# Kernel tuning notes

Hardware: AMD Instinct MI355X
Metric: run time of the kernel (lower is better)

## Reference

```python
import jax, jax.numpy as jnp
import numpy as np

N = 512           # nodes
DIM = 64          # feature dim (in_dim == dim)
KS = (0.9, 0.7, 0.6)
M_DIM = 17
EDGE_DIM = 1
EIN = 2 * DIM + 1 + EDGE_DIM  # EGNN edge-mlp input width = 130
L = 3             # shared EGNN layers per scale


def _rn(k, shape, s=0.05):
    return jax.random.normal(k, shape, jnp.float32) * s


def setup_inputs() -> dict:
    key = jax.random.key(0)
    k = jax.random.split(key, 12)
    feat = jax.random.normal(k[0], (1, N, DIM), jnp.float32)
    coor = jax.random.normal(k[1], (1, N, 3), jnp.float32)
    # sparse-ish binary adjacency stored densely, as the module expects
    edge = (jax.random.uniform(k[2], (1, N, N, 1)) < 0.05).astype(jnp.float32)
    return {
        "feat": feat, "coor": coor, "edge": edge,
        "We1": _rn(k[3], (L, EIN, 2 * EIN)), "be1": jnp.zeros((L, 2 * EIN), jnp.float32),
        "We2": _rn(k[4], (L, 2 * EIN, M_DIM)), "be2": jnp.zeros((L, M_DIM), jnp.float32),
        "Wc1": _rn(k[5], (L, M_DIM, 4 * M_DIM)), "bc1": jnp.zeros((L, 4 * M_DIM), jnp.float32),
        "Wc2": _rn(k[6], (L, 4 * M_DIM, 1)), "bc2": jnp.zeros((L, 1), jnp.float32),
        "Wn1": _rn(k[7], (L, DIM + M_DIM, 2 * DIM)), "bn1": jnp.zeros((L, 2 * DIM), jnp.float32),
        "Wn2": _rn(k[8], (L, 2 * DIM, DIM)), "bn2": jnp.zeros((L, DIM), jnp.float32),
        "wp": _rn(k[9], (len(KS), DIM)), "bp": jnp.zeros((len(KS),), jnp.float32),
        "ep": 0,
    }


def _egnn(feats, coors, edges, We1, be1, We2, be2, Wc1, bc1, Wc2, bc2,
          Wn1, bn1, Wn2, bn2):
    # feats [B,n,d], coors [B,n,3], edges [B,n,n,1]
    rel = coors[:, :, None, :] - coors[:, None, :, :]           # [B,n,n,3]
    dist = jnp.sum(rel * rel, axis=-1, keepdims=True)           # [B,n,n,1]
    B, n, d = feats.shape
    fi = jnp.broadcast_to(feats[:, :, None, :], (B, n, n, d))
    fj = jnp.broadcast_to(feats[:, None, :, :], (B, n, n, d))
    e_in = jnp.concatenate([fi, fj, dist, edges], axis=-1)      # [B,n,n,EIN]
    m = jax.nn.silu(jax.nn.silu(e_in @ We1 + be1) @ We2 + be2)  # [B,n,n,M]
    cw = jax.nn.silu(m @ Wc1 + bc1) @ Wc2 + bc2                 # [B,n,n,1]
    coors_out = coors + jnp.sum(cw * rel, axis=2)               # [B,n,3]
    m_i = jnp.sum(m, axis=2)                                    # [B,n,M]
    h = jax.nn.silu(jnp.concatenate([feats, m_i], axis=-1) @ Wn1 + bn1) @ Wn2 + bn2
    return feats + h, coors_out


def _forward(feat, coor, edge, We1, be1, We2, be2, Wc1, bc1, Wc2, bc2,
             Wn1, bn1, Wn2, bn2, wp, bp):
    org_h, org_g, org_c = feat[0], edge[0, :, :, 0], coor[0]
    n_nodes = org_h.shape[0]
    ug = (org_g != 0).astype(jnp.float32)
    ug2 = ((ug @ ug) != 0).astype(jnp.float32)  # 2-hop closure adjacency
    hs = []
    for i, kf in enumerate(KS):
        kcnt = max(2, int(kf * n_nodes))
        scores = jax.nn.sigmoid(org_h @ wp[i] + bp[i])          # [n]
        vals, idx = jax.lax.top_k(scores, kcnt)
        h = org_h[idx] * vals[:, None]                          # gather + scale
        g = ug2[idx][:, idx]                                    # row+col gather
        c = org_c[idx]
        hc, coors, edges = h[None], c[None], g[None, :, :, None]
        for j in range(3):
            ht, coors = _egnn(hc, coors, edges,
                              We1[j], be1[j], We2[j], be2[j],
                              Wc1[j], bc1[j], Wc2[j], bc2[j],
                              Wn1[j], bn1[j], Wn2[j], bn2[j])
            hc = jax.nn.relu(hc + ht)
        # unpool: zero-scatter back to original node set
        h_full = jnp.zeros((n_nodes, hc.shape[-1]), hc.dtype).at[idx].set(hc[0])
        hs.append(h_full)
    out = hs[-1]
    for h_i in hs:
        out = jnp.maximum(out, h_i)
    return out


def reference(feat, coor, edge, We1, be1, We2, be2, Wc1, bc1, Wc2, bc2,
              Wn1, bn1, Wn2, bn2, wp, bp, ep):
    return _forward(feat, coor, edge, We1, be1, We2, be2, Wc1, bc1, Wc2, bc2,
                    Wn1, bn1, Wn2, bn2, wp, bp)
```

## Files before the change

### kernel.cpp

```cpp
#include <hip/hip_runtime.h>
#include <hip/hip_bf16.h>

typedef unsigned long long u64;
typedef unsigned int u32;
typedef unsigned short u16;

#define NN   512
#define DIMF 64
#define E2   260
#define KPAD 272
#define MD   17
#define MH   68
#define NH1  128
#define K0   460
#define K1   358
#define K2   307
#define KT   1125
#define O1   460
#define O2   818
#define PADU 1152
#define AS   272
#define NT0  8
#define NT1  6
#define NT2  5
#define T0T   (K0*NT0)
#define T01T  (T0T + K1*NT1)
#define TTOT  (T01T + K2*NT2)
#define PBLK  ((TTOT+3)/4)
#define MSTR  40
#define WVLDS 5120

typedef __attribute__((ext_vector_type(8)))  short short8;
typedef __attribute__((ext_vector_type(16))) float f32x16;

union SF  { int4 i4; u16 us[8]; u32 w[4]; short8 v; };
union F4U { float4 v; float2 h[2]; float f[4]; u32 w[4]; };

__device__ __forceinline__ float fast_exp2(float x){
#if __has_builtin(__builtin_amdgcn_exp2f)
    return __builtin_amdgcn_exp2f(x);
#else
    return __expf(x * 0.6931471805599453f);
#endif
}
__device__ __forceinline__ float fast_rcp(float x){
#if __has_builtin(__builtin_amdgcn_rcpf)
    return __builtin_amdgcn_rcpf(x);
#else
    return __fdividef(1.0f, x);
#endif
}
__device__ __forceinline__ float siluf(float x){
    return x * fast_rcp(1.0f + fast_exp2(x * -1.4426950408889634f));
}
__device__ __forceinline__ float sigf(float x){
    return fast_rcp(1.0f + fast_exp2(x * -1.4426950408889634f));
}
__device__ __forceinline__ u16 bf16_rne(float f){
    u32 u = __float_as_uint(f);
    u += 0x7FFFu + ((u >> 16) & 1u);
    return (u16)(u >> 16);
}
__device__ __forceinline__ float bf16f(u16 h){
    return __uint_as_float(((u32)h) << 16);
}
__device__ __forceinline__ u32 pk_bf16(float x, float y){
    float2 f2; f2.x = x; f2.y = y;
    __hip_bfloat162 h = __float22bfloat162_rn(f2);
    union { __hip_bfloat162 b; u32 u; } cv; cv.b = h;
    return cv.u;
}
__device__ __forceinline__ void lgkm_wait(){
#if __has_builtin(__builtin_amdgcn_s_waitcnt)
    __builtin_amdgcn_s_waitcnt(0xC07F);
#endif
}
__device__ __forceinline__ float2 f2add(float2 a, float2 b){ return float2{a.x+b.x, a.y+b.y}; }
__device__ __forceinline__ float2 f2mul(float2 a, float2 b){ return float2{a.x*b.x, a.y*b.y}; }
__device__ __forceinline__ float2 f2fma(float2 a, float2 b, float2 c){
    return float2{fmaf(a.x,b.x,c.x), fmaf(a.y,b.y,c.y)};
}
__device__ __forceinline__ float2 silu2(float2 p){
    float2 t = f2mul(p, float2{-1.4426950408889634f, -1.4426950408889634f});
    float ex = fast_exp2(t.x), ey = fast_exp2(t.y);
    float rx = fast_rcp(1.0f + ex), ry = fast_rcp(1.0f + ey);
    return float2{p.x*rx, p.y*ry};
}

__global__ __launch_bounds__(256) void k_pre(
    const float* __restrict__ edge, const float* __restrict__ feat,
    const float* __restrict__ wp, const float* __restrict__ bp,
    const float* __restrict__ We2, const float* __restrict__ Wc1,
    const float* __restrict__ We1, const float* __restrict__ be2,
    const float* __restrict__ bc1, const float* __restrict__ Wc2,
    u64* __restrict__ ugw, float* __restrict__ scores,
    u16* __restrict__ W2f, u16* __restrict__ Wc1f,
    float* __restrict__ wdP, float* __restrict__ weP, float* __restrict__ be2P,
    float* __restrict__ bc1P, float* __restrict__ Wc2P, u64* __restrict__ ug2w){
    int blk = blockIdx.x, t = threadIdx.x;
    if (blk < 128){
        int i = blk*4 + (t>>6); int lane = t&63;
        const float* row = edge + (size_t)i*NN;
        for (int w = 0; w < 8; w++){
            u64 m = __ballot(row[w*64+lane] != 0.0f);
            if (lane == 0) ugw[i*8+w] = m;
        }
        return;
    }
    if (blk < 134){
        int gid = (blk-128)*256 + t; if (gid >= 3*NN) return;
        int l = gid>>9, n = gid&511;
        float s = bp[l];
        for (int d = 0; d < DIMF; d++) s = fmaf(feat[n*DIMF+d], wp[l*DIMF+d], s);
        scores[gid] = sigf(s);
        return;
    }
    int idx = (blk-134)*256 + t;
    if (idx < 52224){
        int e = idx&7, lane = (idx>>3)&63, hl = (idx>>9)&1, c = (idx>>10)%17, jl = idx/17408;
        int q = lane>>5, nn = lane&31;
        int k = c*16 + q*8 + e;
        float v = (k < E2 && nn < MD) ? We2[jl*E2*MD + k*MD + nn] : 0.0f;
        u16 hi = bf16_rne(v);
        W2f[idx] = hl ? bf16_rne(v - bf16f(hi)) : hi;
        return;
    }
    idx -= 52224;
    if (idx < 9216){
        int e = idx & 7, lane = (idx>>3)&63, c2 = (idx>>9)&1, T = (idx>>10)%3, jl = idx/3072;
        int q = lane>>5, nn = lane&31;
        int o = c2*16 + q*8 + e, h = T*32 + nn;
        float v = (o < MD && h < MH) ? Wc1[jl*MD*MH + o*MH + h] : 0.0f;
        Wc1f[idx] = bf16_rne(v);
        return;
    }
    idx -= 9216;
    if (idx < 816){ int jl = idx/KPAD, k = idx%KPAD;
        wdP[idx] = (k < E2) ? We1[jl*130*E2 + 128*E2 + k] : 0.0f; return; }
    idx -= 816;
    if (idx < 816){ int jl = idx/KPAD, k = idx%KPAD;
        weP[idx] = (k < E2) ? We1[jl*130*E2 + 129*E2 + k] : 0.0f; return; }
    idx -= 816;
    if (idx < 96){ int jl = idx/32, o = idx%32;
        be2P[idx] = (o < MD) ? be2[jl*MD+o] : 0.0f; return; }
    idx -= 96;
    if (idx < 288){ int jl = idx/96, h = idx%96;
        bc1P[idx] = (h < MH) ? bc1[jl*MH+h] : 0.0f; return; }
    idx -= 288;
    if (idx < 288){ int jl = idx/96, h = idx%96;
        Wc2P[idx] = (h < MH) ? Wc2[jl*MH+h] : 0.0f; return; }
    idx -= 288;
    if (idx < 4096){ ug2w[idx] = 0ULL; return; }
}

__global__ __launch_bounds__(512) void k_sortug2(
    const float* __restrict__ scores, const u64* __restrict__ ugw,
    float* __restrict__ svals, int* __restrict__ sidx, int* __restrict__ rev,
    u64* __restrict__ ug2w){
    int blk = blockIdx.x, t = threadIdx.x;
    if (blk < 3){
        int l = blk;
        __shared__ float sk[NN];
        __shared__ int   si[NN];
        sk[t] = scores[l*NN+t]; si[t] = t; rev[l*NN+t] = -1;
        __syncthreads();
        for (int k = 2; k <= NN; k <<= 1){
            for (int jj = k>>1; jj > 0; jj >>= 1){
                int p = t ^ jj;
                if (p > t){
                    float ka = sk[t], kb = sk[p];
                    int ia = si[t], ib = si[p];
                    bool before = (ka > kb) || (ka == kb && ia < ib);
                    bool sw = ((t & k) == 0) ? (!before) : before;
                    if (sw){ sk[t]=kb; sk[p]=ka; si[t]=ib; si[p]=ia; }
                }
                __syncthreads();
            }
        }
        svals[l*NN+t] = sk[t]; sidx[l*NN+t] = si[t];
        int kcnt = (l==0)?K0:(l==1)?K1:K2;
        if (t < kcnt) rev[l*NN + si[t]] = t;
    } else {
        int gid = (blk-3)*512 + t;
        int i  = gid >> 6;
        int w  = (gid >> 3) & 7;
        int kc = gid & 7;
        u64 rm = ugw[i*8 + kc];
        u64 acc = 0;
        int base = kc*64;
        while (rm){
            int k2 = __builtin_ctzll(rm);
            rm &= rm - 1;
            acc |= ugw[(base + k2)*8 + w];
        }
        if (acc) atomicOr(&ug2w[i*8 + w], acc);
    }
}

__device__ __forceinline__ void ab_comp(int jl, const float* __restrict__ We1,
                                        const float* __restrict__ be1, float hval,
                                        int u, int lane,
                                        float* __restrict__ Ap, float* __restrict__ BF){
    const float* W = We1 + jl*130*E2;
    int r  = 4*lane;
    int rt = 256 + lane;
    int rtc = (lane < 4) ? rt : 256;
    F4U av; av.v = *(const float4*)(be1 + jl*E2 + r);
    F4U bv; bv.f[0]=bv.f[1]=bv.f[2]=bv.f[3]=0.0f;
    float avx = be1[jl*E2 + rtc];
    float bvx = 0.0f;
    for (int d = 0; d < DIMF; d++){
        float hv = __shfl(hval, d);
        F4U w1; w1.v = *(const float4*)(W + d*E2 + r);
        F4U w2; w2.v = *(const float4*)(W + (DIMF+d)*E2 + r);
#pragma unroll
        for (int i = 0; i < 4; i++){
            av.f[i] = fmaf(hv, w1.f[i], av.f[i]);
            bv.f[i] = fmaf(hv, w2.f[i], bv.f[i]);
        }
        avx = fmaf(hv, W[d*E2 + rtc], avx);
        bvx = fmaf(hv, W[(DIMF+d)*E2 + rtc], bvx);
    }
    *(float4*)(Ap + u*AS + r) = av.v;
    *(float4*)(BF + ((size_t)(lane>>1)*PADU + u)*8 + (lane&1)*4) = bv.v;
    if (lane < 16){
        int k = 256 + lane;
        float aval = (lane < 4) ? avx : 0.0f;
        float bval = (lane < 4) ? bvx : 0.0f;
        Ap[u*AS + k] = aval;
        BF[((size_t)(k>>3)*PADU + u)*8 + (k&7)] = bval;
    }
}

__global__ __launch_bounds__(256) void k_gab(
    const float* __restrict__ feat, const float* __restrict__ coor,
    const float* __restrict__ svals, const int* __restrict__ sidx,
    const float* __restrict__ We1, const float* __restrict__ be1,
    float* __restrict__ hc, float* __restrict__ c0, float* __restrict__ c1,
    float* __restrict__ mi, float* __restrict__ Ap, float* __restrict__ BF){
    int t = threadIdx.x; int u = blockIdx.x*4 + (t>>6); if (u >= KT) return;
    int lane = t&63;
    int l = (u<K0)?0:(u<O2)?1:2;
    int a = u - ((l==0)?0:(l==1)?O1:O2);
    int org = sidx[l*NN+a];
    float val = svals[l*NN+a];
    float hval = feat[org*DIMF+lane]*val;
    hc[u*DIMF+lane] = hval;
    if (lane < 3){ float c = coor[org*3+lane]; c0[u*4+lane]=c; c1[u*4+lane]=c; }
    if (lane == 3){ c0[u*4+3]=0.0f; c1[u*4+3]=0.0f; }
    if (lane < 20) mi[u*20+lane] = 0.0f;
    ab_comp(0, We1, be1, hval, u, lane, Ap, BF);
}

template<int DOCW>
__global__ __launch_bounds__(256, 4) void k_pair(
    int jl,
    const float* __restrict__ Ap, const float* __restrict__ BF,
    const u16* __restrict__ W2f, const u16* __restrict__ Wc1f,
    const float* __restrict__ wdP, const float* __restrict__ weP,
    const float* __restrict__ be2P, const float* __restrict__ bc1P,
    const float* __restrict__ Wc2P, const float* __restrict__ bc2,
    const float* __restrict__ cin, float* __restrict__ cout,
    float* __restrict__ mi, const int* __restrict__ sidx,
    const u64* __restrict__ ug2w){
    __shared__ __align__(16) char sWK[4*WVLDS];
    __shared__ __align__(16) char sWD[1088];
    __shared__ __align__(16) char sWE[1088];
    int t = threadIdx.x;
    if (t < 68)       ((float4*)sWD)[t]    = *(const float4*)(wdP + jl*KPAD + 4*t);
    else if (t < 136) ((float4*)sWE)[t-68] = *(const float4*)(weP + jl*KPAD + 4*(t-68));
    int wid0 = blockIdx.x*4 + (t>>6);
    int lane = t&63, n = lane&31, q = lane>>5;
    bool dead = (wid0 >= TTOT);
    int wid = dead ? (TTOT-1) : wid0;
    int l, kl, off, a, tile;
    if (wid < T0T)       { l=0; kl=K0; off=0;  a = wid>>3; tile = wid&7; }
    else if (wid < T01T) { int w = wid-T0T;  l=1; kl=K1; off=O1; a = w/NT1; tile = w - a*NT1; }
    else                 { int w = wid-T01T; l=2; kl=K2; off=O2; a = w/NT2; tile = w - a*NT2; }
    int u = off + a;
    int b0 = tile*64 + n, b1 = b0 + 32;
    float act0 = (b0 < kl) ? 1.0f : 0.0f;
    float act1 = (b1 < kl) ? 1.0f : 0.0f;
    int b0c = min(b0, kl-1), b1c = min(b1, kl-1);
    int ub0 = off + b0c, ub1 = off + b1c;
    int ia  = sidx[l*NN+a];
    int ib0 = sidx[l*NN+b0c], ib1 = sidx[l*NN+b1c];
    float ef0 = act0 * (float)((ug2w[ia*8 + (ib0>>6)] >> (ib0&63)) & 1ULL);
    float ef1 = act1 * (float)((ug2w[ia*8 + (ib1>>6)] >> (ib1&63)) & 1ULL);
    F4U ca;  ca.v  = ((const float4*)cin)[u];
    F4U cb0; cb0.v = ((const float4*)cin)[ub0];
    F4U cb1; cb1.v = ((const float4*)cin)[ub1];
    float tx0 = ca.f[0]-cb0.f[0], ty0 = ca.f[1]-cb0.f[1], tz0 = ca.f[2]-cb0.f[2];
    float tx1 = ca.f[0]-cb1.f[0], ty1 = ca.f[1]-cb1.f[1], tz1 = ca.f[2]-cb1.f[2];
    float dd0 = tx0*tx0 + ty0*ty0 + tz0*tz0;
    float dd1 = tx1*tx1 + ty1*ty1 + tz1*tz1;

    char* myk = sWK + (t>>6)*WVLDS;
    {
        const float* Au = Ap + u*AS;
        ((float4*)myk)[lane] = *(const float4*)(Au + 4*lane);
        if (lane < 4) ((float4*)myk)[64+lane] = *(const float4*)(Au + 256 + 4*lane);
    }
    __syncthreads();

    const float* pB0 = BF + ((size_t)q*PADU + ub0)*8;
    const float* pB1 = BF + ((size_t)q*PADU + ub1)*8;
    const u16*   pW  = W2f + jl*17408 + lane*8;
    const char*  pA  = myk + q*32;
    const char*  pWD = sWD + q*32;
    const char*  pWE = sWE + q*32;

    f32x16 acc0, acc1;
#pragma unroll
    for (int r = 0; r < 16; r++){ acc0[r] = 0.0f; acc1[r] = 0.0f; }

    F4U nb0a, nb0b, nb1a, nb1b; SF nwh;
    nb0a.v = *(const float4*)(pB0);     nb0b.v = *(const float4*)(pB0 + 4);
    nb1a.v = *(const float4*)(pB1);     nb1b.v = *(const float4*)(pB1 + 4);
    nwh.i4 = *(const int4*)(pW);

    float2 DD0{dd0,dd0}, EF0{ef0,ef0}, DD1{dd1,dd1}, EF1{ef1,ef1};

    for (int c = 0; c < 17; c++){
        F4U b0a = nb0a, b0b = nb0b, b1a = nb1a, b1b = nb1b;
        SF  wh  = nwh;
        pB0 += 2*PADU*8; pB1 += 2*PADU*8; pW += 1024;
        if (c < 16){
            nb0a.v = *(const float4*)(pB0);     nb0b.v = *(const float4*)(pB0 + 4);
            nb1a.v = *(const float4*)(pB1);     nb1b.v = *(const float4*)(pB1 + 4);
            nwh.i4 = *(const int4*)(pW);
        }
        F4U a0, a1, w0, w1, e0, e1;
        a0.v = *(const float4*)(pA);       a1.v = *(const float4*)(pA + 16);
        w0.v = *(const float4*)(pWD);      w1.v = *(const float4*)(pWD + 16);
        e0.v = *(const float4*)(pWE);      e1.v = *(const float4*)(pWE + 16);
        pA += 64; pWD += 64; pWE += 64;

        SF shi0, shi1;
#pragma unroll
        for (int h = 0; h < 2; h++){
            float2 p00 = f2fma(EF0, e0.h[h], f2fma(DD0, w0.h[h], f2add(a0.h[h], b0a.h[h])));
            float2 p01 = f2fma(EF0, e1.h[h], f2fma(DD0, w1.h[h], f2add(a1.h[h], b0b.h[h])));
            float2 p10 = f2fma(EF1, e0.h[h], f2fma(DD1, w0.h[h], f2add(a0.h[h], b1a.h[h])));
            float2 p11 = f2fma(EF1, e1.h[h], f2fma(DD1, w1.h[h], f2add(a1.h[h], b1b.h[h])));
            float2 s00 = silu2(p00), s01 = silu2(p01);
            float2 s10 = silu2(p10), s11 = silu2(p11);
            shi0.w[h]   = pk_bf16(s00.x, s00.y);
            shi0.w[2+h] = pk_bf16(s01.x, s01.y);
            shi1.w[h]   = pk_bf16(s10.x, s10.y);
            shi1.w[2+h] = pk_bf16(s11.x, s11.y);
        }
        acc0 = __builtin_amdgcn_mfma_f32_32x32x16_bf16(shi0.v, wh.v, acc0, 0, 0, 0);
        acc1 = __builtin_amdgcn_mfma_f32_32x32x16_bf16(shi1.v, wh.v, acc1, 0, 0, 0);
    }

    float be2v = be2P[jl*32 + n];
    u16* mlds = (u16*)myk;
    float msum = 0.0f;
#pragma unroll
    for (int r = 0; r < 16; r++){
        int row = (r&3) + 8*(r>>2) + 4*q;
        float m0 = siluf(acc0[r] + be2v);
        float m1 = siluf(acc1[r] + be2v);
        m0 = (tile*64 + row      < kl) ? m0 : 0.0f;
        m1 = (tile*64 + 32 + row < kl) ? m1 : 0.0f;
        msum += m0 + m1;
        if (DOCW){
            mlds[row*MSTR + n]        = bf16_rne(m0);
            mlds[(row+32)*MSTR + n]   = bf16_rne(m1);
        }
    }
    msum += __shfl_xor(msum, 32);
    if (!dead && lane < MD) atomicAdd(&mi[u*20 + lane], msum);

    if (DOCW){
        lgkm_wait();
        const char* mb = (const char*)mlds;
        float gx = 0.0f, gy = 0.0f, gz = 0.0f;
        float bc2v = bc2[jl];
#pragma unroll
        for (int S = 0; S < 2; S++){
            SF af0, af1;
            af0.i4 = *(const int4*)(mb + (S*32+n)*(MSTR*2) + q*16);
            af1.i4 = *(const int4*)(mb + (S*32+n)*(MSTR*2) + 32 + q*16);
            float cwp[16];
#pragma unroll
            for (int r = 0; r < 16; r++) cwp[r] = 0.0f;
            for (int T = 0; T < 3; T++){
                SF bb0, bb1;
                bb0.i4 = *(const int4*)(Wc1f + jl*3072 + T*1024 +       lane*8);
                bb1.i4 = *(const int4*)(Wc1f + jl*3072 + T*1024 + 512 + lane*8);
                f32x16 p2;
#pragma unroll
                for (int r = 0; r < 16; r++) p2[r] = 0.0f;
                p2 = __builtin_amdgcn_mfma_f32_32x32x16_bf16(af0.v, bb0.v, p2, 0, 0, 0);
                p2 = __builtin_amdgcn_mfma_f32_32x32x16_bf16(af1.v, bb1.v, p2, 0, 0, 0);
                float bc1v = bc1P[jl*96 + T*32 + n];
                float wc2v = Wc2P[jl*96 + T*32 + n];
#pragma unroll
                for (int r = 0; r < 16; r++)
                    cwp[r] = fmaf(siluf(p2[r] + bc1v), wc2v, cwp[r]);
            }
#pragma unroll
            for (int r = 0; r < 16; r++){
                int row  = (r&3) + 8*(r>>2) + 4*q + S*32;
                int brow = tile*64 + row;
                F4U cbr; cbr.v = ((const float4*)cin)[off + min(brow, kl-1)];
                float cw = cwp[r] + ((n == 0) ? bc2v : 0.0f);
                cw = (brow < kl) ? cw : 0.0f;
                gx = fmaf(cw, ca.f[0]-cbr.f[0], gx);
                gy = fmaf(cw, ca.f[1]-cbr.f[1], gy);
                gz = fmaf(cw, ca.f[2]-cbr.f[2], gz);
            }
        }
#pragma unroll
        for (int s = 1; s < 64; s <<= 1){
            gx += __shfl_xor(gx, s); gy += __shfl_xor(gy, s); gz += __shfl_xor(gz, s);
        }
        if (!dead && lane == 0){
            atomicAdd(&cout[u*4+0], gx);
            atomicAdd(&cout[u*4+1], gy);
            atomicAdd(&cout[u*4+2], gz);
        }
    }
}

__global__ __launch_bounds__(256) void k_nodeab(
    int jl, int donext, int docopy,
    const float* __restrict__ Wn1, const float* __restrict__ bn1,
    const float* __restrict__ Wn2, const float* __restrict__ bn2,
    const float* __restrict__ We1, const float* __restrict__ be1,
    float* __restrict__ hc, float* __restrict__ mi,
    const float* __restrict__ ccur, float* __restrict__ cnext,
    float* __restrict__ Ap, float* __restrict__ BF){
    int t = threadIdx.x; int u = blockIdx.x*4 + (t>>6); if (u >= KT) return;
    int lane = t&63;
    float hval = hc[u*DIMF+lane];
    float mval = (lane < MD) ? mi[u*20+lane] : 0.0f;
    const float* W1 = Wn1 + jl*(DIMF+MD)*NH1;
    float v0 = bn1[jl*NH1+lane], v1 = bn1[jl*NH1+lane+64];
    for (int d = 0; d < DIMF; d++){
        float x = __shfl(hval, d);
        v0 = fmaf(x, W1[d*NH1+lane],    v0);
        v1 = fmaf(x, W1[d*NH1+lane+64], v1);
    }
    for (int d = 0; d < MD; d++){
        float x = __shfl(mval, d);
        v0 = fmaf(x, W1[(DIMF+d)*NH1+lane],    v0);
        v1 = fmaf(x, W1[(DIMF+d)*NH1+lane+64], v1);
    }
    float s0 = siluf(v0), s1 = siluf(v1);
    const float* W2 = Wn2 + jl*NH1*DIMF;
    float h = bn2[jl*DIMF+lane];
    for (int i = 0; i < 64; i++) h = fmaf(__shfl(s0, i), W2[i*DIMF+lane], h);
    for (int i = 0; i < 64; i++) h = fmaf(__shfl(s1, i), W2[(64+i)*DIMF+lane], h);
    float hn = fmaxf(0.0f, fmaf(2.0f, hval, h));
    hc[u*DIMF+lane] = hn;
    if (donext){
        if (lane < 20) mi[u*20+lane] = 0.0f;
        if (docopy && lane < 4) cnext[u*4+lane] = ccur[u*4+lane];
        ab_comp(jl+1, We1, be1, hn, u, lane, Ap, BF);
    }
}

__global__ void k_final(const float* __restrict__ hc, const int* __restrict__ rev,
                        float* __restrict__ out){
    int gid = blockIdx.x*blockDim.x + threadIdx.x;
    if (gid >= NN*DIMF) return;
    int nn = gid>>6, d = gid&63;
    float v = 0.0f;
    int a0 = rev[0*NN+nn]; if (a0 >= 0) v = fmaxf(v, hc[(0  + a0)*DIMF + d]);
    int a1 = rev[1*NN+nn]; if (a1 >= 0) v = fmaxf(v, hc[(O1 + a1)*DIMF + d]);
    int a2 = rev[2*NN+nn]; if (a2 >= 0) v = fmaxf(v, hc[(O2 + a2)*DIMF + d]);
    out[gid] = v;
}

extern "C" void kernel_launch(void* const* d_in, const int* in_sizes, int n_in,
                              void* d_out, int out_size, void* d_ws, size_t ws_size,
                              hipStream_t stream) {
    (void)in_sizes; (void)n_in; (void)out_size; (void)ws_size;
    const float* feat = (const float*)d_in[0];
    const float* coor = (const float*)d_in[1];
    const float* edge = (const float*)d_in[2];
    const float* We1  = (const float*)d_in[3];
    const float* be1  = (const float*)d_in[4];
    const float* We2  = (const float*)d_in[5];
    const float* be2  = (const float*)d_in[6];
    const float* Wc1  = (const float*)d_in[7];
    const float* bc1  = (const float*)d_in[8];
    const float* Wc2  = (const float*)d_in[9];
    const float* bc2  = (const float*)d_in[10];
    const float* Wn1  = (const float*)d_in[11];
    const float* bn1  = (const float*)d_in[12];
    const float* Wn2  = (const float*)d_in[13];
    const float* bn2  = (const float*)d_in[14];
    const float* wp   = (const float*)d_in[15];
    const float* bp   = (const float*)d_in[16];
    float* out = (float*)d_out;

    char* wsb = (char*)d_ws;
    u64*   ugw    = (u64*)  (wsb + 0);
    u64*   ug2w   = (u64*)  (wsb + 32768);
    float* scores = (float*)(wsb + 65536);
    float* svals  = (float*)(wsb + 71680);
    int*   sidx   = (int*)  (wsb + 77824);
    int*   rev    = (int*)  (wsb + 83968);
    float* c0     = (float*)(wsb + 90112);
    float* c1     = (float*)(wsb + 108544);
    float* mi     = (float*)(wsb + 126976);
    float* hc     = (float*)(wsb + 217088);
    float* Ap     = (float*)(wsb + 505344);
    float* BF     = (float*)(wsb + 1729536);
    u16*   W2f    = (u16*)  (wsb + 2982912);
    u16*   Wc1f   = (u16*)  (wsb + 3087360);
    float* wdP    = (float*)(wsb + 3105792);
    float* weP    = (float*)(wsb + 3109120);
    float* be2P   = (float*)(wsb + 3112448);
    float* bc1P   = (float*)(wsb + 3112832);
    float* Wc2P   = (float*)(wsb + 3113984);

    k_pre<<<399, 256, 0, stream>>>(edge, feat, wp, bp, We2, Wc1, We1, be2, bc1, Wc2,
                                   ugw, scores, W2f, Wc1f,
                                   wdP, weP, be2P, bc1P, Wc2P, ug2w);
    k_sortug2<<<67, 512, 0, stream>>>(scores, ugw, svals, sidx, rev, ug2w);
    k_gab<<<282, 256, 0, stream>>>(feat, coor, svals, sidx, We1, be1,
                                   hc, c0, c1, mi, Ap, BF);
    k_pair<1><<<PBLK, 256, 0, stream>>>(0, Ap, BF, W2f, Wc1f,
                                        wdP, weP, be2P, bc1P, Wc2P, bc2,
                                        c0, c1, mi, sidx, ug2w);
    k_nodeab<<<282, 256, 0, stream>>>(0, 1, 1, Wn1, bn1, Wn2, bn2, We1, be1,
                                      hc, mi, c1, c0, Ap, BF);
    k_pair<1><<<PBLK, 256, 0, stream>>>(1, Ap, BF, W2f, Wc1f,
                                        wdP, weP, be2P, bc1P, Wc2P, bc2,
                                        c1, c0, mi, sidx, ug2w);
    k_nodeab<<<282, 256, 0, stream>>>(1, 1, 0, Wn1, bn1, Wn2, bn2, We1, be1,
                                      hc, mi, c0, c1, Ap, BF);
    k_pair<0><<<PBLK, 256, 0, stream>>>(2, Ap, BF, W2f, Wc1f,
                                        wdP, weP, be2P, bc1P, Wc2P, bc2,
                                        c0, c1, mi, sidx, ug2w);
    k_nodeab<<<282, 256, 0, stream>>>(2, 0, 0, Wn1, bn1, Wn2, bn2, We1, be1,
                                      hc, mi, c0, c1, Ap, BF);
    k_final<<<128, 256, 0, stream>>>(hc, rev, out);
}
```

Baseline: 373.6 us.

## Split per-node MLP and edge projection work across two wavefronts per node

k_gab and k_nodeab now give each node two 64-lane wavefronts instead of one. Each wave computes half of the node-MLP hidden units and half of the We1 projection columns. Partial results of the second node-MLP layer are exchanged through shared memory with block barriers. This doubles the grid so latency-bound per-node matvecs have more waves in flight, at the cost of extra syncs, shared-memory traffic and duplicated input loads.

```diff
diff --git a/kernel.cpp b/kernel.cpp
--- a/kernel.cpp
+++ b/kernel.cpp
@@ -27,6 +27,7 @@
 #define T01T  (T0T + K1*NT1)
 #define TTOT  (T01T + K2*NT2)
 #define PBLK  ((TTOT+3)/4)
+#define GB2   ((KT+1)/2)
 #define MSTR  40
 #define WVLDS 5120
 
@@ -197,38 +198,39 @@
     }
 }
 
-__device__ __forceinline__ void ab_comp(int jl, const float* __restrict__ We1,
-                                        const float* __restrict__ be1, float hval,
-                                        int u, int lane,
-                                        float* __restrict__ Ap, float* __restrict__ BF){
+__device__ __forceinline__ void ab_comp2(int jl, const float* __restrict__ We1,
+                                         const float* __restrict__ be1, float hval,
+                                         int u, int lane, int w, bool dead,
+                                         float* __restrict__ Ap, float* __restrict__ BF){
     const float* W = We1 + jl*130*E2;
-    int r  = 4*lane;
-    int rt = 256 + lane;
-    int rtc = (lane < 4) ? rt : 256;
-    F4U av; av.v = *(const float4*)(be1 + jl*E2 + r);
-    F4U bv; bv.f[0]=bv.f[1]=bv.f[2]=bv.f[3]=0.0f;
+    int r  = w*128 + 2*lane;
+    int rt = 256 + w*2 + lane;
+    int rtc = (lane < 2) ? rt : 256;
+    float2 av = *(const float2*)(be1 + jl*E2 + r);
+    float2 bv = {0.0f, 0.0f};
     float avx = be1[jl*E2 + rtc];
     float bvx = 0.0f;
     for (int d = 0; d < DIMF; d++){
         float hv = __shfl(hval, d);
-        F4U w1; w1.v = *(const float4*)(W + d*E2 + r);
-        F4U w2; w2.v = *(const float4*)(W + (DIMF+d)*E2 + r);
-#pragma unroll
-        for (int i = 0; i < 4; i++){
-            av.f[i] = fmaf(hv, w1.f[i], av.f[i]);
-            bv.f[i] = fmaf(hv, w2.f[i], bv.f[i]);
-        }
+        float2 w1 = *(const float2*)(W + d*E2 + r);
+        float2 w2 = *(const float2*)(W + (DIMF+d)*E2 + r);
+        av.x = fmaf(hv, w1.x, av.x); av.y = fmaf(hv, w1.y, av.y);
+        bv.x = fmaf(hv, w2.x, bv.x); bv.y = fmaf(hv, w2.y, bv.y);
         avx = fmaf(hv, W[d*E2 + rtc], avx);
         bvx = fmaf(hv, W[(DIMF+d)*E2 + rtc], bvx);
     }
-    *(float4*)(Ap + u*AS + r) = av.v;
-    *(float4*)(BF + ((size_t)(lane>>1)*PADU + u)*8 + (lane&1)*4) = bv.v;
-    if (lane < 16){
-        int k = 256 + lane;
-        float aval = (lane < 4) ? avx : 0.0f;
-        float bval = (lane < 4) ? bvx : 0.0f;
-        Ap[u*AS + k] = aval;
-        BF[((size_t)(k>>3)*PADU + u)*8 + (k&7)] = bval;
+    if (!dead){
+        *(float2*)(Ap + u*AS + r) = av;
+        *(float2*)(BF + ((size_t)(r>>3)*PADU + u)*8 + (r&7)) = bv;
+        if (lane < 2){
+            Ap[u*AS + rt] = avx;
+            BF[((size_t)(rt>>3)*PADU + u)*8 + (rt&7)] = bvx;
+        }
+        if (lane >= 2 && lane < 8){
+            int k = 260 + w*6 + (lane-2);
+            Ap[u*AS + k] = 0.0f;
+            BF[((size_t)(k>>3)*PADU + u)*8 + (k&7)] = 0.0f;
+        }
     }
 }
 
@@ -238,18 +240,22 @@
     const float* __restrict__ We1, const float* __restrict__ be1,
     float* __restrict__ hc, float* __restrict__ c0, float* __restrict__ c1,
     float* __restrict__ mi, float* __restrict__ Ap, float* __restrict__ BF){
-    int t = threadIdx.x; int u = blockIdx.x*4 + (t>>6); if (u >= KT) return;
-    int lane = t&63;
+    int t = threadIdx.x;
+    int g = t>>7, w = (t>>6)&1, lane = t&63;
+    int u = blockIdx.x*2 + g;
+    if (u >= KT) return;
     int l = (u<K0)?0:(u<O2)?1:2;
     int a = u - ((l==0)?0:(l==1)?O1:O2);
     int org = sidx[l*NN+a];
     float val = svals[l*NN+a];
     float hval = feat[org*DIMF+lane]*val;
-    hc[u*DIMF+lane] = hval;
-    if (lane < 3){ float c = coor[org*3+lane]; c0[u*4+lane]=c; c1[u*4+lane]=c; }
-    if (lane == 3){ c0[u*4+3]=0.0f; c1[u*4+3]=0.0f; }
-    if (lane < 20) mi[u*20+lane] = 0.0f;
-    ab_comp(0, We1, be1, hval, u, lane, Ap, BF);
+    if (w == 0){
+        hc[u*DIMF+lane] = hval;
+        if (lane < 3){ float c = coor[org*3+lane]; c0[u*4+lane]=c; c1[u*4+lane]=c; }
+        if (lane == 3){ c0[u*4+3]=0.0f; c1[u*4+3]=0.0f; }
+        if (lane < 20) mi[u*20+lane] = 0.0f;
+    }
+    ab_comp2(0, We1, be1, hval, u, lane, w, false, Ap, BF);
 }
 
 template<int DOCW>
@@ -433,33 +439,38 @@
     float* __restrict__ hc, float* __restrict__ mi,
     const float* __restrict__ ccur, float* __restrict__ cnext,
     float* __restrict__ Ap, float* __restrict__ BF){
-    int t = threadIdx.x; int u = blockIdx.x*4 + (t>>6); if (u >= KT) return;
-    int lane = t&63;
+    __shared__ float sbuf[2][NH1];
+    __shared__ float hpart[2][2][DIMF];
+    int t = threadIdx.x;
+    int g = t>>7, w = (t>>6)&1, lane = t&63;
+    int u0 = blockIdx.x*2 + g;
+    bool dead = (u0 >= KT);
+    int u = dead ? (KT-1) : u0;
     float hval = hc[u*DIMF+lane];
     float mval = (lane < MD) ? mi[u*20+lane] : 0.0f;
     const float* W1 = Wn1 + jl*(DIMF+MD)*NH1;
-    float v0 = bn1[jl*NH1+lane], v1 = bn1[jl*NH1+lane+64];
-    for (int d = 0; d < DIMF; d++){
-        float x = __shfl(hval, d);
-        v0 = fmaf(x, W1[d*NH1+lane],    v0);
-        v1 = fmaf(x, W1[d*NH1+lane+64], v1);
-    }
-    for (int d = 0; d < MD; d++){
-        float x = __shfl(mval, d);
-        v0 = fmaf(x, W1[(DIMF+d)*NH1+lane],    v0);
-        v1 = fmaf(x, W1[(DIMF+d)*NH1+lane+64], v1);
-    }
-    float s0 = siluf(v0), s1 = siluf(v1);
+    int oc = w*64 + lane;
+    float v = bn1[jl*NH1 + oc];
+    for (int d = 0; d < DIMF; d++) v = fmaf(__shfl(hval, d), W1[d*NH1 + oc], v);
+    for (int d = 0; d < MD;  d++) v = fmaf(__shfl(mval, d), W1[(DIMF+d)*NH1 + oc], v);
+    sbuf[g][oc] = siluf(v);
+    __syncthreads();
     const float* W2 = Wn2 + jl*NH1*DIMF;
-    float h = bn2[jl*DIMF+lane];
-    for (int i = 0; i < 64; i++) h = fmaf(__shfl(s0, i), W2[i*DIMF+lane], h);
-    for (int i = 0; i < 64; i++) h = fmaf(__shfl(s1, i), W2[(64+i)*DIMF+lane], h);
-    float hn = fmaxf(0.0f, fmaf(2.0f, hval, h));
-    hc[u*DIMF+lane] = hn;
+    float h = (w == 0) ? bn2[jl*DIMF + lane] : 0.0f;
+    for (int i = 0; i < 64; i++){
+        int idx = w*64 + i;
+        h = fmaf(sbuf[g][idx], W2[idx*DIMF + lane], h);
+    }
+    hpart[g][w][lane] = h;
+    __syncthreads();
+    float hn = fmaxf(0.0f, fmaf(2.0f, hval, hpart[g][0][lane] + hpart[g][1][lane]));
+    if (!dead && w == 0) hc[u*DIMF + lane] = hn;
     if (donext){
-        if (lane < 20) mi[u*20+lane] = 0.0f;
-        if (docopy && lane < 4) cnext[u*4+lane] = ccur[u*4+lane];
-        ab_comp(jl+1, We1, be1, hn, u, lane, Ap, BF);
+        if (!dead && w == 0){
+            if (lane < 20) mi[u*20 + lane] = 0.0f;
+            if (docopy && lane < 4) cnext[u*4 + lane] = ccur[u*4 + lane];
+        }
+        ab_comp2(jl+1, We1, be1, hn, u, lane, w, dead, Ap, BF);
     }
 }
 
@@ -523,22 +534,22 @@
                                    ugw, scores, W2f, Wc1f,
                                    wdP, weP, be2P, bc1P, Wc2P, ug2w);
     k_sortug2<<<67, 512, 0, stream>>>(scores, ugw, svals, sidx, rev, ug2w);
-    k_gab<<<282, 256, 0, stream>>>(feat, coor, svals, sidx, We1, be1,
+    k_gab<<<GB2, 256, 0, stream>>>(feat, coor, svals, sidx, We1, be1,
                                    hc, c0, c1, mi, Ap, BF);
     k_pair<1><<<PBLK, 256, 0, stream>>>(0, Ap, BF, W2f, Wc1f,
                                         wdP, weP, be2P, bc1P, Wc2P, bc2,
                                         c0, c1, mi, sidx, ug2w);
-    k_nodeab<<<282, 256, 0, stream>>>(0, 1, 1, Wn1, bn1, Wn2, bn2, We1, be1,
+    k_nodeab<<<GB2, 256, 0, stream>>>(0, 1, 1, Wn1, bn1, Wn2, bn2, We1, be1,
                                       hc, mi, c1, c0, Ap, BF);
     k_pair<1><<<PBLK, 256, 0, stream>>>(1, Ap, BF, W2f, Wc1f,
                                         wdP, weP, be2P, bc1P, Wc2P, bc2,
                                         c1, c0, mi, sidx, ug2w);
-    k_nodeab<<<282, 256, 0, stream>>>(1, 1, 0, Wn1, bn1, Wn2, bn2, We1, be1,
+    k_nodeab<<<GB2, 256, 0, stream>>>(1, 1, 0, Wn1, bn1, Wn2, bn2, We1, be1,
                                       hc, mi, c0, c1, Ap, BF);
     k_pair<0><<<PBLK, 256, 0, stream>>>(2, Ap, BF, W2f, Wc1f,
                                         wdP, weP, be2P, bc1P, Wc2P, bc2,
                                         c0, c1, mi, sidx, ug2w);
-    k_nodeab<<<282, 256, 0, stream>>>(2, 0, 0, Wn1, bn1, Wn2, bn2, We1, be1,
+    k_nodeab<<<GB2, 256, 0, stream>>>(2, 0, 0, Wn1, bn1, Wn2, bn2, We1, be1,
                                       hc, mi, c0, c1, Ap, BF);
     k_final<<<128, 256, 0, stream>>>(hc, rev, out);
 }
```

Measured after the change: 381.7 us. +2.2%, slower.
